# Kernel optimization log

Measured on AMD Instinct MI355X. Metric: run time of the kernel, lower is better.

## Reference

```python
import jax, jax.numpy as jnp
import numpy as np

B, T, D = 2, 2048, 1024
H = 16
HD = D // H
WINDOW = 128
N_GLOBAL = 1
SCALE = 1.0 / np.sqrt(HD)


def _attend_mask(T):
    # True = allowed to attend: banded local window + global rows/cols
    idx = jnp.arange(T)
    dist = jnp.abs(idx[:, None] - idx[None, :])
    attend = dist <= WINDOW
    glb = idx < N_GLOBAL
    attend = attend | glb[:, None] | glb[None, :]
    return attend  # [T, T] bool


def setup_inputs() -> dict:
    key = jax.random.key(0)
    ks = jax.random.split(key, 5)
    scale_w = 1.0 / np.sqrt(D)
    return {
        "x": jax.random.normal(ks[0], (B, T, D), dtype=jnp.float32),
        "Wq": jax.random.normal(ks[1], (D, D), dtype=jnp.float32) * scale_w,
        "Wk": jax.random.normal(ks[2], (D, D), dtype=jnp.float32) * scale_w,
        "Wv": jax.random.normal(ks[3], (D, D), dtype=jnp.float32) * scale_w,
        "Wo": jax.random.normal(ks[4], (D, D), dtype=jnp.float32) * scale_w,
    }


def reference(x, Wq, Wk, Wv, Wo):
    Bb, Tt, Dd = x.shape
    # torch nn.Linear: y = x @ W.T
    q = (x @ Wq.T).reshape(Bb, Tt, H, HD).transpose(0, 2, 1, 3)  # [B,H,T,hd]
    k = (x @ Wk.T).reshape(Bb, Tt, H, HD).transpose(0, 2, 1, 3)
    v = (x @ Wv.T).reshape(Bb, Tt, H, HD).transpose(0, 2, 1, 3)

    attend = _attend_mask(Tt)  # [T,T]
    logits = jnp.einsum("bhqd,bhkd->bhqk", q, k) * SCALE
    logits = jnp.where(attend[None, None, :, :], logits, -jnp.inf)
    weights = jax.nn.softmax(logits, axis=-1)
    weights = jnp.nan_to_num(weights)
    out = jnp.einsum("bhqk,bhkd->bhqd", weights, v)
    out = out.transpose(0, 2, 1, 3).reshape(Bb, Tt, Dd)
    return out @ Wo.T
```

## Files before the change

### kernel.cpp

```cpp
#include <hip/hip_runtime.h>

typedef unsigned short u16;
typedef __attribute__((ext_vector_type(8))) __bf16 bf16x8;
typedef __attribute__((ext_vector_type(4))) float f32x4;
typedef __attribute__((ext_vector_type(8))) u16 u16x8;

#define T_SEQ 2048
#define DIM   1024
#define HDIM  64
#define WIN   128
#define XN_EL (2 * T_SEQ * DIM)

#define AS1 __attribute__((address_space(1)))
#define AS3 __attribute__((address_space(3)))

__device__ __forceinline__ u16 f2bf(float f) {
  union { float f; unsigned u; } v; v.f = f;
  unsigned r = v.u + 0x7fffu + ((v.u >> 16) & 1u);
  return (u16)(r >> 16);
}
__device__ __forceinline__ float bf2f(u16 u) {
  union { unsigned u; float f; } v; v.u = ((unsigned)u) << 16; return v.f;
}
__device__ __forceinline__ void bar() {
  asm volatile("" ::: "memory");
  __builtin_amdgcn_s_barrier();
  asm volatile("" ::: "memory");
}

__global__ __launch_bounds__(256) void cvt_all(
    const float* __restrict__ x,  const float* __restrict__ wq,
    const float* __restrict__ wk, const float* __restrict__ wv,
    const float* __restrict__ wo, u16* __restrict__ xb, u16* __restrict__ wb) {
  const int bid = blockIdx.x;
  const float* s;
  u16* d;
  int off;
  if (bid < 2048) {
    s = x; d = xb; off = bid * 2048;
  } else {
    const int w = bid - 2048;
    const int m = w >> 9;
    s = (m == 0) ? wq : ((m == 1) ? wk : ((m == 2) ? wv : wo));
    d = wb + ((size_t)m << 20);
    off = (w & 511) * 2048;
  }
  const int i = off + threadIdx.x * 8;
  const float4* s4 = (const float4*)(s + i);
  float4 a = s4[0], b = s4[1];
  u16x8 r;
  r[0] = f2bf(a.x); r[1] = f2bf(a.y); r[2] = f2bf(a.z); r[3] = f2bf(a.w);
  r[4] = f2bf(b.x); r[5] = f2bf(b.y); r[6] = f2bf(b.z); r[7] = f2bf(b.w);
  *(u16x8*)(d + i) = r;
}

__global__ __launch_bounds__(512, 2) void gemm8(
    const u16* __restrict__ A, const u16* __restrict__ B,
    u16* __restrict__ C, int nbm) {
  constexpr int NT = 16;
  __shared__ u16 As[2][256 * 64];
  __shared__ u16 Bs[2][192 * 64];

  const int tid = threadIdx.x;
  const int lane = tid & 63;
  const int wid = tid >> 6;
  const int wr = wid >> 2, wc = wid & 3;
  const int c15 = lane & 15, g = lane >> 4;
  const int lr = lane >> 3;
  const int lcs = ((lane & 7) ^ lr) << 3;

  const int cpx = gridDim.x >> 3;
  const int bid = ((int)blockIdx.x & 7) * cpx + ((int)blockIdx.x >> 3);
  const int bm = bid % nbm;
  const int nb = bid / nbm;
  const u16* Ab = A + (size_t)bm * 256 * DIM;
  const u16* Bb = B + (size_t)nb * 192 * DIM;

  f32x4 acc[8][3];
#pragma unroll
  for (int m = 0; m < 8; ++m)
#pragma unroll
    for (int n = 0; n < 3; ++n) acc[m][n] = (f32x4){0.f, 0.f, 0.f, 0.f};

  auto stAh = [&](int buf, int half, int t) {
    const int k0 = t * 64;
#pragma unroll
    for (int i = 0; i < 2; ++i) {
      const int c = half * 16 + wid * 2 + i;
      __builtin_amdgcn_global_load_lds(
          (const AS1 void*)(Ab + (size_t)(c * 8 + lr) * DIM + k0 + lcs),
          (AS3 void*)(&As[buf][c * 512]), 16, 0, 0);
    }
  };
  auto stBt = [&](int buf, int third, int t) {
    const int k0 = t * 64;
    const int c = third * 8 + wid;
    __builtin_amdgcn_global_load_lds(
        (const AS1 void*)(Bb + (size_t)(c * 8 + lr) * DIM + k0 + lcs),
        (AS3 void*)(&Bs[buf][c * 512]), 16, 0, 0);
  };

  stAh(0, 0, 0); stAh(0, 1, 0);
  stBt(0, 0, 0); stBt(0, 1, 0); stBt(0, 2, 0);
  stBt(1, 0, 1); stBt(1, 1, 1); stBt(1, 2, 1);
  asm volatile("s_waitcnt vmcnt(3)" ::: "memory");
  bar();

  for (int t2 = 0; t2 < NT; t2 += 2) {
    bf16x8 bfrag[3][2];
#pragma unroll
    for (int p = 0; p < 8; ++p) {
      const int q = p & 3;
      const int buf = (p >> 2);
      if (q == 0) {
#pragma unroll
        for (int n = 0; n < 3; ++n)
#pragma unroll
          for (int ks = 0; ks < 2; ++ks) {
            const int r = wc * 48 + n * 16 + c15;
            bfrag[n][ks] = *(const bf16x8*)(
                &Bs[buf][r * 64 + ((ks * 32 + g * 8) ^ ((r & 7) << 3))]);
          }
      }
      bf16x8 af[2][2];
#pragma unroll
      for (int m = 0; m < 2; ++m)
#pragma unroll
        for (int ks = 0; ks < 2; ++ks) {
          const int r = wr * 128 + (q * 2 + m) * 16 + c15;
          af[m][ks] = *(const bf16x8*)(
              &As[buf][r * 64 + ((ks * 32 + g * 8) ^ ((r & 7) << 3))]);
        }
      const bool s2 = (t2 + 2) < NT;
      const bool s3 = (t2 + 3) < NT;
      if (p == 0) {
        stAh(1, 0, t2 + 1);
      } else if (p == 1) {
        stAh(1, 1, t2 + 1);
        if (s2) stBt(0, 0, t2 + 2);
      } else if (p == 2) {
        if (s2) stBt(0, 1, t2 + 2);
      } else if (p == 3) {
        if (s2) { stBt(0, 2, t2 + 2);
                  asm volatile("s_waitcnt vmcnt(3)" ::: "memory"); }
        else    { asm volatile("s_waitcnt vmcnt(0)" ::: "memory"); }
      } else if (p == 4) {
        if (s2) stAh(0, 0, t2 + 2);
      } else if (p == 5) {
        if (s2) stAh(0, 1, t2 + 2);
        if (s3) stBt(1, 0, t2 + 3);
      } else if (p == 6) {
        if (s3) stBt(1, 1, t2 + 3);
      } else {
        if (s3) { stBt(1, 2, t2 + 3);
                  asm volatile("s_waitcnt vmcnt(3)" ::: "memory"); }
        else if (s2) { asm volatile("s_waitcnt vmcnt(0)" ::: "memory"); }
      }
      bar();
      __builtin_amdgcn_s_setprio(1);
#pragma unroll
      for (int m = 0; m < 2; ++m)
#pragma unroll
        for (int n = 0; n < 3; ++n)
#pragma unroll
          for (int ks = 0; ks < 2; ++ks)
            acc[q * 2 + m][n] = __builtin_amdgcn_mfma_f32_16x16x32_bf16(
                af[m][ks], bfrag[n][ks], acc[q * 2 + m][n], 0, 0, 0);
      __builtin_amdgcn_s_setprio(0);
      bar();
    }
  }

#pragma unroll
  for (int m = 0; m < 8; ++m) {
    const int row0 = bm * 256 + wr * 128 + m * 16 + g * 4;
#pragma unroll
    for (int n = 0; n < 3; ++n) {
      const int col = nb * 192 + wc * 48 + n * 16 + c15;
#pragma unroll
      for (int j = 0; j < 4; ++j) {
        u16* dst = C + (size_t)(col >> 10) * (size_t)XN_EL +
                   (col & 1023) + (size_t)(row0 + j) * DIM;
        *dst = f2bf(acc[m][n][j]);
      }
    }
  }
}

template <int BM, int BN, int WM, int WN, int OS, typename OUT_T>
__global__ __launch_bounds__(WM * WN * 64, 2) void gemm3(
    const u16* __restrict__ A, const u16* __restrict__ B,
    OUT_T* __restrict__ C, int nbm) {
  constexpr int NW = WM * WN;
  constexpr int RM = BM / WM, RN = BN / WN;
  constexpr int MF = RM / 16, NF = RN / 16;
  constexpr int MPH = MF / 4;
  constexpr int NT = DIM / 64;
  constexpr int CA = BM / 8, CB = BN / 8;
  constexpr int ANW = CA / NW;
  constexpr int BNW = CB / NW;

  __shared__ u16 As[2][BM * 64];
  __shared__ u16 Bs[2][BN * 64];

  const int tid = threadIdx.x;
  const int lane = tid & 63;
  const int wid = tid >> 6;
  const int wr = wid / WN, wc = wid % WN;
  const int c15 = lane & 15, g = lane >> 4;
  const int lr = lane >> 3;
  const int lcs = ((lane & 7) ^ lr) << 3;

  const int cpx = gridDim.x >> 3;
  const int bid = ((int)blockIdx.x & 7) * cpx + ((int)blockIdx.x >> 3);
  const int bm = bid % nbm;
  const int nb = bid / nbm;
  const u16* Ab = A + (size_t)bm * BM * DIM;
  const u16* Bb = B + (size_t)nb * BN * DIM;

  f32x4 acc[MF][NF];
#pragma unroll
  for (int m = 0; m < MF; ++m)
#pragma unroll
    for (int n = 0; n < NF; ++n) acc[m][n] = (f32x4){0.f, 0.f, 0.f, 0.f};

  auto stA = [&](int buf, int half, int k0) {
#pragma unroll
    for (int i = 0; i < ANW / 2; ++i) {
      const int c = half * (CA / 2) + wid * (ANW / 2) + i;
      __builtin_amdgcn_global_load_lds(
          (const AS1 void*)(Ab + (size_t)(c * 8 + lr) * DIM + k0 + lcs),
          (AS3 void*)(&As[buf][c * 512]), 16, 0, 0);
    }
  };
  auto stB = [&](int buf, int k0) {
#pragma unroll
    for (int i = 0; i < BNW; ++i) {
      const int c = wid * BNW + i;
      __builtin_amdgcn_global_load_lds(
          (const AS1 void*)(Bb + (size_t)(c * 8 + lr) * DIM + k0 + lcs),
          (AS3 void*)(&Bs[buf][c * 512]), 16, 0, 0);
    }
  };

  stA(0, 0, 0); stA(0, 1, 0);
  stB(0, 0); stB(1, 64);
  asm volatile("s_waitcnt vmcnt(4)" ::: "memory");
  bar();

  for (int t = 0; t < NT; ++t) {
    const int buf = t & 1;
    const int k0 = t * 64;
    bf16x8 bfrag[NF][2];
#pragma unroll
    for (int p = 0; p < 4; ++p) {
      if (p == 0) {
#pragma unroll
        for (int n = 0; n < NF; ++n)
#pragma unroll
          for (int ks = 0; ks < 2; ++ks) {
            const int r = wc * RN + n * 16 + c15;
            bfrag[n][ks] = *(const bf16x8*)(
                &Bs[buf][r * 64 + ((ks * 32 + g * 8) ^ ((r & 7) << 3))]);
          }
      }
      bf16x8 af[MPH][2];
#pragma unroll
      for (int m = 0; m < MPH; ++m)
#pragma unroll
        for (int ks = 0; ks < 2; ++ks) {
          const int r = wr * RM + (p * MPH + m) * 16 + c15;
          af[m][ks] = *(const bf16x8*)(
              &As[buf][r * 64 + ((ks * 32 + g * 8) ^ ((r & 7) << 3))]);
        }
      if (p == 0) {
        if (t + 1 < NT) stA(buf ^ 1, 0, k0 + 64);
      } else if (p == 1) {
        if (t + 1 < NT) stA(buf ^ 1, 1, k0 + 64);
      } else if (p == 2) {
        if (t + 2 < NT) stB(buf, k0 + 128);
      } else {
        if (t < NT - 2) asm volatile("s_waitcnt vmcnt(4)" ::: "memory");
        else            asm volatile("s_waitcnt vmcnt(0)" ::: "memory");
      }
      bar();
      __builtin_amdgcn_s_setprio(1);
#pragma unroll
      for (int m = 0; m < MPH; ++m)
#pragma unroll
        for (int n = 0; n < NF; ++n)
#pragma unroll
          for (int ks = 0; ks < 2; ++ks)
            acc[p * MPH + m][n] = __builtin_amdgcn_mfma_f32_16x16x32_bf16(
                af[m][ks], bfrag[n][ks], acc[p * MPH + m][n], 0, 0, 0);
      __builtin_amdgcn_s_setprio(0);
      bar();
    }
  }

#pragma unroll
  for (int m = 0; m < MF; ++m) {
    const int row0 = bm * BM + wr * RM + m * 16 + g * 4;
#pragma unroll
    for (int n = 0; n < NF; ++n) {
      const int col = nb * BN + wc * RN + n * 16 + c15;
#pragma unroll
      for (int j = 0; j < 4; ++j) {
        const size_t idx = (size_t)(row0 + j) * OS + col;
        if constexpr (sizeof(OUT_T) == 2) C[idx] = f2bf(acc[m][n][j]);
        else C[idx] = acc[m][n][j];
      }
    }
  }
}

__global__ __launch_bounds__(256) void sparse_attn(
    const u16* __restrict__ Q, const u16* __restrict__ K,
    const u16* __restrict__ V, u16* __restrict__ AO) {
  __shared__ u16 Ks[64 * 72];
  __shared__ u16 Vt[64 * 72];
  __shared__ u16 Pl[4][16 * 72];
  __shared__ float Pg[4][16];

  const int tid = threadIdx.x;
  const int lane = tid & 63;
  const int wid = tid >> 6;

  const int id = blockIdx.x;
  const int xcd = id & 7;
  const int slot = id >> 3;
  const int pl = slot / 33;
  const int within = slot % 33;
  const int pair = xcd * 4 + pl;
  const int by = pair & 15;
  const int bz = pair >> 4;

  const size_t ha = (size_t)bz * T_SEQ * DIM + (size_t)by * HDIM;
  const u16* Qp = Q + ha;
  const u16* Kp = K + ha;
  const u16* Vp = V + ha;

  if (within == 0) {
    float* qs   = (float*)Pg;
    float* ps   = (float*)Ks;
    float* rbuf = (float*)Vt;
    float* red  = (float*)(&Pl[0][0]);

    if (tid < HDIM) qs[tid] = bf2f(Qp[tid]);
    __syncthreads();

    float lsum = 0.f;
#pragma unroll
    for (int j = 0; j < 8; ++j) {
      const int k = tid + 256 * j;
      const u16* kr = Kp + (size_t)k * DIM;
      float acc = 0.f;
#pragma unroll
      for (int d0 = 0; d0 < 8; ++d0) {
        u16x8 kv = *(const u16x8*)(kr + d0 * 8);
#pragma unroll
        for (int e = 0; e < 8; ++e) acc += qs[d0 * 8 + e] * bf2f(kv[e]);
      }
      const float p = __expf(acc * 0.125f);
      ps[k] = p;
      lsum += p;
    }
#pragma unroll
    for (int s = 1; s < 64; s <<= 1) lsum += __shfl_xor(lsum, s);
    if (lane == 0) red[wid] = lsum;
    __syncthreads();
    const float denom = red[0] + red[1] + red[2] + red[3];

    const int kg = tid >> 3, dg = tid & 7;
    float facc[8] = {0.f, 0.f, 0.f, 0.f, 0.f, 0.f, 0.f, 0.f};
#pragma unroll 8
    for (int i = 0; i < 64; ++i) {
      const int k = kg * 64 + i;
      const u16x8 vv = *(const u16x8*)(Vp + (size_t)k * DIM + dg * 8);
      const float p = ps[k];
#pragma unroll
      for (int e = 0; e < 8; ++e) facc[e] += p * bf2f(vv[e]);
    }
#pragma unroll
    for (int e = 0; e < 8; ++e) rbuf[kg * 64 + dg * 8 + e] = facc[e];
    __syncthreads();
    if (tid < HDIM) {
      float tot = 0.f;
#pragma unroll
      for (int k2 = 0; k2 < 32; ++k2) tot += rbuf[k2 * 64 + tid];
      AO[ha + tid] = f2bf(tot / denom);
    }
    return;
  }

  const int c15 = lane & 15;
  const int g = lane >> 4;
  const int q0 = (within - 1) * 64;
  const int r0 = q0 + wid * 16;

  bf16x8 qf0, qf1;
  {
    const u16* qp = Qp + (size_t)(r0 + c15) * DIM + g * 8;
    qf0 = *(const bf16x8*)qp;
    qf1 = *(const bf16x8*)(qp + 32);
  }

  float lrun[4] = {0.f, 0.f, 0.f, 0.f};
  f32x4 ao[4];
#pragma unroll
  for (int c = 0; c < 4; ++c) ao[c] = (f32x4){0.f, 0.f, 0.f, 0.f};

  const int klo = (q0 > WIN) ? (q0 - WIN) : 0;
  int khi = q0 + 64 + WIN;
  if (khi > T_SEQ) khi = T_SEQ;
  const int nt = (khi - klo) >> 6;

  const int srr = tid >> 2;
  const int scc = (tid & 3) * 16;
  const int vr = srr ^ (scc & 48);

  const u16* kbase = Kp + (size_t)(klo + srr) * DIM + scc;
  const u16* vbase = Vp + (size_t)(klo + srr) * DIM + scc;
  u16x8 kp0 = *(const u16x8*)kbase;
  u16x8 kp1 = *(const u16x8*)(kbase + 8);
  u16x8 vp0 = *(const u16x8*)vbase;
  u16x8 vp1 = *(const u16x8*)(vbase + 8);

  for (int ti = 0; ti < nt; ++ti) {
    const int kt = klo + ti * 64;
    *(u16x8*)(Ks + srr * 72 + scc) = kp0;
    *(u16x8*)(Ks + srr * 72 + scc + 8) = kp1;
#pragma unroll
    for (int e = 0; e < 8; ++e) {
      Vt[(scc + e) * 72 + vr] = vp0[e];
      Vt[(scc + 8 + e) * 72 + vr] = vp1[e];
    }
    __syncthreads();

    if (ti + 1 < nt) {
      const u16* kn = kbase + (size_t)(ti + 1) * 64 * DIM;
      const u16* vn = vbase + (size_t)(ti + 1) * 64 * DIM;
      kp0 = *(const u16x8*)kn;
      kp1 = *(const u16x8*)(kn + 8);
      vp0 = *(const u16x8*)vn;
      vp1 = *(const u16x8*)(vn + 8);
    }

    f32x4 s[4];
#pragma unroll
    for (int t = 0; t < 4; ++t) {
      const u16* kr = Ks + (t * 16 + c15) * 72 + g * 8;
      bf16x8 ka = *(const bf16x8*)kr;
      bf16x8 kb = *(const bf16x8*)(kr + 32);
      f32x4 z = (f32x4){0.f, 0.f, 0.f, 0.f};
      z = __builtin_amdgcn_mfma_f32_16x16x32_bf16(qf0, ka, z, 0, 0, 0);
      s[t] = __builtin_amdgcn_mfma_f32_16x16x32_bf16(qf1, kb, z, 0, 0, 0);
    }
    if (kt >= r0 - 113 && kt <= r0 + 65) {
#pragma unroll
      for (int j = 0; j < 4; ++j) {
#pragma unroll
        for (int t = 0; t < 4; ++t) {
          const float p = __expf(s[t][j] * 0.125f);
          lrun[j] += p;
          Pl[wid][(g * 4 + j) * 72 + t * 16 + c15] = f2bf(p);
        }
      }
    } else {
#pragma unroll
      for (int j = 0; j < 4; ++j) {
        const int qg = r0 + g * 4 + j;
#pragma unroll
        for (int t = 0; t < 4; ++t) {
          const int kg = kt + t * 16 + c15;
          const int dd = qg - kg;
          const bool ok = (kg == 0) || (dd <= WIN && dd >= -WIN);
          const float p = ok ? __expf(s[t][j] * 0.125f) : 0.f;
          lrun[j] += p;
          Pl[wid][(g * 4 + j) * 72 + t * 16 + c15] = f2bf(p);
        }
      }
    }
    asm volatile("s_waitcnt lgkmcnt(0)" ::: "memory");

    const bf16x8 pa0 = *(const bf16x8*)(&Pl[wid][c15 * 72 + g * 8]);
    const bf16x8 pa1 = *(const bf16x8*)(&Pl[wid][c15 * 72 + 32 + g * 8]);
#pragma unroll
    for (int c = 0; c < 4; ++c) {
      const int rb = (c * 16 + c15) * 72;
      bf16x8 va = *(const bf16x8*)(Vt + rb + ((g * 8) ^ (c << 4)));
      bf16x8 vb = *(const bf16x8*)(Vt + rb + ((32 + g * 8) ^ (c << 4)));
      ao[c] = __builtin_amdgcn_mfma_f32_16x16x32_bf16(pa0, va, ao[c], 0, 0, 0);
      ao[c] = __builtin_amdgcn_mfma_f32_16x16x32_bf16(pa1, vb, ao[c], 0, 0, 0);
    }
    __syncthreads();
  }

  float ltot[4];
#pragma unroll
  for (int j = 0; j < 4; ++j) {
    float ls = lrun[j];
    ls += __shfl_xor(ls, 1);
    ls += __shfl_xor(ls, 2);
    ls += __shfl_xor(ls, 4);
    ls += __shfl_xor(ls, 8);
    ltot[j] = ls;
  }

  if (klo > 0) {
    const u16x8 qu0 = *(const u16x8*)&qf0;
    const u16x8 qu1 = *(const u16x8*)&qf1;
    const u16x8 k0a = *(const u16x8*)(Kp + g * 8);
    const u16x8 k0b = *(const u16x8*)(Kp + 32 + g * 8);
    float sg = 0.f;
#pragma unroll
    for (int e = 0; e < 8; ++e)
      sg += bf2f(qu0[e]) * bf2f(k0a[e]) + bf2f(qu1[e]) * bf2f(k0b[e]);
    sg += __shfl_xor(sg, 16);
    sg += __shfl_xor(sg, 32);
    const float pg = __expf(sg * 0.125f);
    Pg[wid][c15] = pg;
    asm volatile("s_waitcnt lgkmcnt(0)" ::: "memory");
#pragma unroll
    for (int j = 0; j < 4; ++j) {
      const float pj = Pg[wid][g * 4 + j];
      ltot[j] += pj;
#pragma unroll
      for (int c = 0; c < 4; ++c)
        ao[c][j] += pj * bf2f(Vp[c * 16 + c15]);
    }
  }

#pragma unroll
  for (int j = 0; j < 4; ++j) {
    const int qrow = r0 + g * 4 + j;
    if (qrow == 0) continue;
    const float inv = 1.0f / ltot[j];
#pragma unroll
    for (int c = 0; c < 4; ++c)
      AO[ha + (size_t)qrow * DIM + c * 16 + c15] = f2bf(ao[c][j] * inv);
  }
}

extern "C" void kernel_launch(void* const* d_in, const int* in_sizes, int n_in,
                              void* d_out, int out_size, void* d_ws, size_t ws_size,
                              hipStream_t stream) {
  const float* x  = (const float*)d_in[0];
  const float* Wq = (const float*)d_in[1];
  const float* Wk = (const float*)d_in[2];
  const float* Wv = (const float*)d_in[3];
  const float* Wo = (const float*)d_in[4];
  float* out = (float*)d_out;

  const int WN = DIM * DIM;

  u16* ws  = (u16*)d_ws;
  u16* xb  = ws;
  u16* wb  = ws + (size_t)XN_EL;
  u16* Wob = wb + (size_t)3 * WN;
  u16* Qb  = wb + (size_t)4 * WN;
  u16* Kb  = Qb + (size_t)XN_EL;
  u16* Vb  = Kb + (size_t)XN_EL;

  cvt_all<<<4096, 256, 0, stream>>>(x, Wq, Wk, Wv, Wo, xb, wb);

  gemm8<<<256, 512, 0, stream>>>(xb, wb, Qb, 16);

  sparse_attn<<<1056, 256, 0, stream>>>(Qb, Kb, Vb, xb);

  gemm3<128, 128, 2, 2, DIM, float><<<256, 256, 0, stream>>>(xb, Wob, out, 32);
}
```

Measured before the change: 98.82 us.

## Double-buffer K/V shared tiles in sparse attention to drop one barrier per tile

The K and V shared-memory tiles are now double-buffered. The next tile is written into the alternate buffer after the current tile's MFMAs, and global prefetch runs two tiles ahead, so each iteration needs one __syncthreads instead of two. The aim is to cut barrier stalls and overlap LDS stores with compute. It doubles LDS use for K/V, which may lower occupancy, and it keeps more prefetch registers live.

Measured after the change: 98.83 us. No clear change (+0.0%).

```diff
diff --git a/kernel.cpp b/kernel.cpp
--- a/kernel.cpp
+++ b/kernel.cpp
@@ -317,8 +317,8 @@
 __global__ __launch_bounds__(256) void sparse_attn(
     const u16* __restrict__ Q, const u16* __restrict__ K,
     const u16* __restrict__ V, u16* __restrict__ AO) {
-  __shared__ u16 Ks[64 * 72];
-  __shared__ u16 Vt[64 * 72];
+  __shared__ u16 Ks[2][64 * 72];
+  __shared__ u16 Vt[2][64 * 72];
   __shared__ u16 Pl[4][16 * 72];
   __shared__ float Pg[4][16];
 
@@ -342,8 +342,8 @@
 
   if (within == 0) {
     float* qs   = (float*)Pg;
-    float* ps   = (float*)Ks;
-    float* rbuf = (float*)Vt;
+    float* ps   = (float*)(&Ks[0][0]);
+    float* rbuf = (float*)(&Vt[0][0]);
     float* red  = (float*)(&Pl[0][0]);
 
     if (tid < HDIM) qs[tid] = bf2f(Qp[tid]);
@@ -421,35 +421,36 @@
 
   const u16* kbase = Kp + (size_t)(klo + srr) * DIM + scc;
   const u16* vbase = Vp + (size_t)(klo + srr) * DIM + scc;
+
   u16x8 kp0 = *(const u16x8*)kbase;
   u16x8 kp1 = *(const u16x8*)(kbase + 8);
   u16x8 vp0 = *(const u16x8*)vbase;
   u16x8 vp1 = *(const u16x8*)(vbase + 8);
+  *(u16x8*)(&Ks[0][srr * 72 + scc]) = kp0;
+  *(u16x8*)(&Ks[0][srr * 72 + scc + 8]) = kp1;
+#pragma unroll
+  for (int e = 0; e < 8; ++e) {
+    Vt[0][(scc + e) * 72 + vr] = vp0[e];
+    Vt[0][(scc + 8 + e) * 72 + vr] = vp1[e];
+  }
+  if (nt > 1) {
+    const u16* kn = kbase + (size_t)64 * DIM;
+    const u16* vn = vbase + (size_t)64 * DIM;
+    kp0 = *(const u16x8*)kn;
+    kp1 = *(const u16x8*)(kn + 8);
+    vp0 = *(const u16x8*)vn;
+    vp1 = *(const u16x8*)(vn + 8);
+  }
+  __syncthreads();
 
   for (int ti = 0; ti < nt; ++ti) {
     const int kt = klo + ti * 64;
-    *(u16x8*)(Ks + srr * 72 + scc) = kp0;
-    *(u16x8*)(Ks + srr * 72 + scc + 8) = kp1;
-#pragma unroll
-    for (int e = 0; e < 8; ++e) {
-      Vt[(scc + e) * 72 + vr] = vp0[e];
-      Vt[(scc + 8 + e) * 72 + vr] = vp1[e];
-    }
-    __syncthreads();
-
-    if (ti + 1 < nt) {
-      const u16* kn = kbase + (size_t)(ti + 1) * 64 * DIM;
-      const u16* vn = vbase + (size_t)(ti + 1) * 64 * DIM;
-      kp0 = *(const u16x8*)kn;
-      kp1 = *(const u16x8*)(kn + 8);
-      vp0 = *(const u16x8*)vn;
-      vp1 = *(const u16x8*)(vn + 8);
-    }
+    const int buf = ti & 1;
 
     f32x4 s[4];
 #pragma unroll
     for (int t = 0; t < 4; ++t) {
-      const u16* kr = Ks + (t * 16 + c15) * 72 + g * 8;
+      const u16* kr = &Ks[buf][(t * 16 + c15) * 72 + g * 8];
       bf16x8 ka = *(const bf16x8*)kr;
       bf16x8 kb = *(const bf16x8*)(kr + 32);
       f32x4 z = (f32x4){0.f, 0.f, 0.f, 0.f};
@@ -488,12 +489,30 @@
 #pragma unroll
     for (int c = 0; c < 4; ++c) {
       const int rb = (c * 16 + c15) * 72;
-      bf16x8 va = *(const bf16x8*)(Vt + rb + ((g * 8) ^ (c << 4)));
-      bf16x8 vb = *(const bf16x8*)(Vt + rb + ((32 + g * 8) ^ (c << 4)));
+      bf16x8 va = *(const bf16x8*)(&Vt[buf][rb + ((g * 8) ^ (c << 4))]);
+      bf16x8 vb = *(const bf16x8*)(&Vt[buf][rb + ((32 + g * 8) ^ (c << 4))]);
       ao[c] = __builtin_amdgcn_mfma_f32_16x16x32_bf16(pa0, va, ao[c], 0, 0, 0);
       ao[c] = __builtin_amdgcn_mfma_f32_16x16x32_bf16(pa1, vb, ao[c], 0, 0, 0);
     }
-    __syncthreads();
+
+    if (ti + 1 < nt) {
+      *(u16x8*)(&Ks[buf ^ 1][srr * 72 + scc]) = kp0;
+      *(u16x8*)(&Ks[buf ^ 1][srr * 72 + scc + 8]) = kp1;
+#pragma unroll
+      for (int e = 0; e < 8; ++e) {
+        Vt[buf ^ 1][(scc + e) * 72 + vr] = vp0[e];
+        Vt[buf ^ 1][(scc + 8 + e) * 72 + vr] = vp1[e];
+      }
+      if (ti + 2 < nt) {
+        const u16* kn = kbase + (size_t)(ti + 2) * 64 * DIM;
+        const u16* vn = vbase + (size_t)(ti + 2) * 64 * DIM;
+        kp0 = *(const u16x8*)kn;
+        kp1 = *(const u16x8*)(kn + 8);
+        vp0 = *(const u16x8*)vn;
+        vp1 = *(const u16x8*)(vn + 8);
+      }
+      __syncthreads();
+    }
   }
 
   float ltot[4];
```
